# Performance work log

Hardware: AMD Instinct MI355X
Metric: run time of the kernel (lower is better)

Reference implementation:

```python
import jax, jax.numpy as jnp
import numpy as np

ALPHA = 1.0
GAMMA = 2.0
LABEL_SMOOTHING = 0.1
CENTER_W = 0.1
B, C = 32768, 1000


def setup_inputs() -> dict:
    key = jax.random.key(0)
    k1, k2 = jax.random.split(key)
    inputs = jax.random.normal(k1, (B, C), dtype=jnp.float32)
    targets = jax.random.randint(k2, (B,), 0, C, dtype=jnp.int64)
    return {"inputs": inputs, "targets": targets}


def reference(inputs, targets):
    n_classes = inputs.shape[1]
    # --- cross entropy with label smoothing (reduction='none') ---
    logp = jax.nn.log_softmax(inputs, axis=-1)                      # [B, C]
    nll = -jnp.take_along_axis(logp, targets[:, None], axis=1)[:, 0]  # [B]
    smooth = -jnp.mean(logp, axis=-1)                               # [B]
    ce = (1.0 - LABEL_SMOOTHING) * nll + LABEL_SMOOTHING * smooth
    # --- focal weighting ---
    pt = jnp.exp(-ce)
    focal = ALPHA * (1.0 - pt) ** GAMMA * ce                        # [B]
    # --- center loss (single-pass segment reduce, no per-class loop) ---
    # torch code sets centers[b, t_b] = mean_i{inputs[i, t_b] : targets[i]==t_b},
    # zero elsewhere.  sum((x - centers)^2) expands to three cheap reductions.
    gathered = jnp.take_along_axis(inputs, targets[:, None], axis=1)[:, 0]  # [B]
    sums = jax.ops.segment_sum(gathered, targets, num_segments=n_classes)
    counts = jax.ops.segment_sum(jnp.ones_like(gathered), targets,
                                 num_segments=n_classes)
    class_mean = jnp.where(counts > 0, sums / jnp.maximum(counts, 1.0), 0.0)
    m = class_mean[targets]                                          # [B]
    n_elems = inputs.shape[0] * inputs.shape[1]
    center = (jnp.sum(inputs ** 2) - 2.0 * jnp.sum(gathered * m)
              + jnp.sum(m ** 2)) / n_elems                           # scalar
    total = focal + CENTER_W * center                                # broadcast scalar
    return total.mean()
```

## Files before the change

kernel.cpp:

```cpp
#include <hip/hip_runtime.h>
#include <cmath>

#define BB 32768
#define CC 1000
#define NF4 250
#define NBLK 8192

__device__ __forceinline__ float wave_reduce_sum(float v) {
  #pragma unroll
  for (int m = 32; m >= 1; m >>= 1) v += __shfl_xor(v, m, 64);
  return v;
}
__device__ __forceinline__ float wave_reduce_max(float v) {
  #pragma unroll
  for (int m = 32; m >= 1; m >>= 1) v = fmaxf(v, __shfl_xor(v, m, 64));
  return v;
}

__global__ __launch_bounds__(256) void hfl_rows(
    const float* __restrict__ x, const int* __restrict__ tgt,
    float* __restrict__ class_sum, float* __restrict__ class_cnt,
    float* __restrict__ pfocal, float* __restrict__ ps2) {
  const int wave = threadIdx.x >> 6;
  const int lane = threadIdx.x & 63;
  const int row  = (blockIdx.x << 2) + wave;

  const float4* rp = reinterpret_cast<const float4*>(x + (size_t)row * CC);
  const int t = tgt[row];

  float4 v[4];
  bool valid[4];
  float vmax = -INFINITY;
  #pragma unroll
  for (int k = 0; k < 4; ++k) {
    const int f4 = (k << 6) + lane;
    valid[k] = (f4 < NF4);
    if (valid[k]) {
      v[k] = rp[f4];
      vmax = fmaxf(vmax, fmaxf(fmaxf(v[k].x, v[k].y), fmaxf(v[k].z, v[k].w)));
    }
  }
  const float rowmax = wave_reduce_max(vmax);

  float se = 0.f, s = 0.f, s2 = 0.f, g = 0.f;
  #pragma unroll
  for (int k = 0; k < 4; ++k) {
    if (valid[k]) {
      const int c0 = (((k << 6) + lane) << 2);
      const float a = v[k].x, b = v[k].y, c = v[k].z, d = v[k].w;
      se += __expf(a - rowmax) + __expf(b - rowmax)
          + __expf(c - rowmax) + __expf(d - rowmax);
      s  += (a + b) + (c + d);
      s2 += (a * a + b * b) + (c * c + d * d);
      if (t >= c0 && t < c0 + 4) {
        const int dd = t - c0;
        g = (dd == 0) ? a : (dd == 1) ? b : (dd == 2) ? c : d;
      }
    }
  }
  se = wave_reduce_sum(se);
  s  = wave_reduce_sum(s);
  s2 = wave_reduce_sum(s2);
  g  = wave_reduce_sum(g);

  __shared__ float sh_f[4], sh_s2[4];
  if (lane == 0) {
    const float lse = rowmax + __logf(se);
    const float ce  = lse - 0.9f * g - 0.1f * (s * (1.0f / CC));
    const float pt  = __expf(-ce);
    const float omp = 1.0f - pt;
    sh_f[wave]  = omp * omp * ce;
    sh_s2[wave] = s2;
    atomicAdd(&class_sum[t], g);
    atomicAdd(&class_cnt[t], 1.0f);
  }
  __syncthreads();
  if (threadIdx.x == 0) {
    pfocal[blockIdx.x] = (sh_f[0] + sh_f[1]) + (sh_f[2] + sh_f[3]);
    ps2[blockIdx.x]    = (sh_s2[0] + sh_s2[1]) + (sh_s2[2] + sh_s2[3]);
  }
}

__global__ __launch_bounds__(1024) void hfl_final(
    const float* __restrict__ class_sum, const float* __restrict__ class_cnt,
    const float* __restrict__ pfocal, const float* __restrict__ ps2,
    float* __restrict__ out) {
  const int tid = threadIdx.x;
  float f = 0.f, s2 = 0.f, ct = 0.f;
  #pragma unroll 2
  for (int i = tid; i < NBLK; i += 1024) { f += pfocal[i]; s2 += ps2[i]; }
  for (int c = tid; c < CC; c += 1024) {
    const float cnt = class_cnt[c];
    if (cnt > 0.f) {
      const float sm = class_sum[c];
      const float m  = sm / cnt;
      ct += 2.0f * m * sm - cnt * m * m;
    }
  }
  f  = wave_reduce_sum(f);
  s2 = wave_reduce_sum(s2);
  ct = wave_reduce_sum(ct);

  __shared__ float shf[16], shs[16], shc[16];
  const int wave = tid >> 6, lane = tid & 63;
  if (lane == 0) { shf[wave] = f; shs[wave] = s2; shc[wave] = ct; }
  __syncthreads();
  if (tid == 0) {
    float F = 0.f, S = 0.f, T = 0.f;
    #pragma unroll
    for (int w = 0; w < 16; ++w) { F += shf[w]; S += shs[w]; T += shc[w]; }
    const float center = (S - T) * (1.0f / ((float)BB * (float)CC));
    out[0] = F * (1.0f / (float)BB) + 0.1f * center;
  }
}

extern "C" void kernel_launch(void* const* d_in, const int* in_sizes, int n_in,
                              void* d_out, int out_size, void* d_ws, size_t ws_size,
                              hipStream_t stream) {
  const float* x   = (const float*)d_in[0];
  const int*   tgt = (const int*)d_in[1];
  float* out = (float*)d_out;

  float* class_sum = (float*)d_ws;
  float* class_cnt = (float*)((char*)d_ws + 4096);
  float* pfocal    = (float*)((char*)d_ws + 8192);
  float* ps2       = (float*)((char*)d_ws + 8192 + NBLK * 4);

  hipMemsetAsync(d_ws, 0, 8192, stream);

  hfl_rows<<<NBLK, 256, 0, stream>>>(x, tgt, class_sum, class_cnt, pfocal, ps2);
  hfl_final<<<1, 1024, 0, stream>>>(class_sum, class_cnt, pfocal, ps2, out);
}
```

Before: 36.09 us.

## Fuse final reduction into row kernel via last-block counter, process 4 rows per wave

Merges the separate single-block final kernel into the row kernel using an atomic block counter, so the last finishing block does the global reduction. Each wave now handles four rows instead of one, which cuts the grid to 2048 blocks and the number of partial sums. The class-center term is simplified algebraically to sum^2/count. This removes one kernel launch and its tail latency, but each wave now runs its four rows one after another, and the last block adds a serialized reduction at the end.

```diff
diff --git a/kernel.cpp b/kernel.cpp
--- a/kernel.cpp
+++ b/kernel.cpp
@@ -4,7 +4,7 @@
 #define BB 32768
 #define CC 1000
 #define NF4 250
-#define NBLK 8192
+#define NBLK 2048
 
 __device__ __forceinline__ float wave_reduce_sum(float v) {
   #pragma unroll
@@ -17,98 +17,107 @@
   return v;
 }
 
-__global__ __launch_bounds__(256) void hfl_rows(
+__global__ __launch_bounds__(256) void hfl_fused(
     const float* __restrict__ x, const int* __restrict__ tgt,
     float* __restrict__ class_sum, float* __restrict__ class_cnt,
-    float* __restrict__ pfocal, float* __restrict__ ps2) {
+    unsigned int* __restrict__ counter,
+    float* __restrict__ pfocal, float* __restrict__ ps2,
+    float* __restrict__ out) {
   const int wave = threadIdx.x >> 6;
   const int lane = threadIdx.x & 63;
-  const int row  = (blockIdx.x << 2) + wave;
 
-  const float4* rp = reinterpret_cast<const float4*>(x + (size_t)row * CC);
-  const int t = tgt[row];
+  float facc = 0.f, s2acc = 0.f;
 
-  float4 v[4];
-  bool valid[4];
-  float vmax = -INFINITY;
   #pragma unroll
-  for (int k = 0; k < 4; ++k) {
-    const int f4 = (k << 6) + lane;
-    valid[k] = (f4 < NF4);
-    if (valid[k]) {
-      v[k] = rp[f4];
-      vmax = fmaxf(vmax, fmaxf(fmaxf(v[k].x, v[k].y), fmaxf(v[k].z, v[k].w)));
-    }
-  }
-  const float rowmax = wave_reduce_max(vmax);
+  for (int j = 0; j < 4; ++j) {
+    const int row = (blockIdx.x << 4) + (wave << 2) + j;
+    const float4* rp = reinterpret_cast<const float4*>(x + (size_t)row * CC);
+    const int t = tgt[row];
 
-  float se = 0.f, s = 0.f, s2 = 0.f, g = 0.f;
-  #pragma unroll
-  for (int k = 0; k < 4; ++k) {
-    if (valid[k]) {
-      const int c0 = (((k << 6) + lane) << 2);
-      const float a = v[k].x, b = v[k].y, c = v[k].z, d = v[k].w;
-      se += __expf(a - rowmax) + __expf(b - rowmax)
-          + __expf(c - rowmax) + __expf(d - rowmax);
-      s  += (a + b) + (c + d);
-      s2 += (a * a + b * b) + (c * c + d * d);
-      if (t >= c0 && t < c0 + 4) {
-        const int dd = t - c0;
-        g = (dd == 0) ? a : (dd == 1) ? b : (dd == 2) ? c : d;
+    float4 v[4];
+    bool valid[4];
+    float vmax = -INFINITY;
+    #pragma unroll
+    for (int k = 0; k < 4; ++k) {
+      const int f4 = (k << 6) + lane;
+      valid[k] = (f4 < NF4);
+      if (valid[k]) {
+        v[k] = rp[f4];
+        vmax = fmaxf(vmax, fmaxf(fmaxf(v[k].x, v[k].y), fmaxf(v[k].z, v[k].w)));
       }
     }
-  }
-  se = wave_reduce_sum(se);
-  s  = wave_reduce_sum(s);
-  s2 = wave_reduce_sum(s2);
-  g  = wave_reduce_sum(g);
+    const float rowmax = wave_reduce_max(vmax);
 
-  __shared__ float sh_f[4], sh_s2[4];
-  if (lane == 0) {
+    float se = 0.f, s = 0.f, s2 = 0.f, g = 0.f;
+    #pragma unroll
+    for (int k = 0; k < 4; ++k) {
+      if (valid[k]) {
+        const int c0 = (((k << 6) + lane) << 2);
+        const float a = v[k].x, b = v[k].y, c = v[k].z, d = v[k].w;
+        se += __expf(a - rowmax) + __expf(b - rowmax)
+            + __expf(c - rowmax) + __expf(d - rowmax);
+        s  += (a + b) + (c + d);
+        s2 += (a * a + b * b) + (c * c + d * d);
+        if (t >= c0 && t < c0 + 4) {
+          const int dd = t - c0;
+          g = (dd == 0) ? a : (dd == 1) ? b : (dd == 2) ? c : d;
+        }
+      }
+    }
+    se = wave_reduce_sum(se);
+    s  = wave_reduce_sum(s);
+    s2 = wave_reduce_sum(s2);
+    g  = wave_reduce_sum(g);
+
     const float lse = rowmax + __logf(se);
     const float ce  = lse - 0.9f * g - 0.1f * (s * (1.0f / CC));
     const float pt  = __expf(-ce);
     const float omp = 1.0f - pt;
-    sh_f[wave]  = omp * omp * ce;
-    sh_s2[wave] = s2;
-    atomicAdd(&class_sum[t], g);
-    atomicAdd(&class_cnt[t], 1.0f);
+    facc  += omp * omp * ce;
+    s2acc += s2;
+    if (lane == 0) {
+      atomicAdd(&class_sum[t], g);
+      atomicAdd(&class_cnt[t], 1.0f);
+    }
   }
+
+  __shared__ float sh_f[4], sh_s2[4];
+  __shared__ int is_last;
+  if (lane == 0) { sh_f[wave] = facc; sh_s2[wave] = s2acc; }
   __syncthreads();
   if (threadIdx.x == 0) {
     pfocal[blockIdx.x] = (sh_f[0] + sh_f[1]) + (sh_f[2] + sh_f[3]);
     ps2[blockIdx.x]    = (sh_s2[0] + sh_s2[1]) + (sh_s2[2] + sh_s2[3]);
+    __threadfence();
+    const unsigned int old = atomicAdd(counter, 1u);
+    is_last = (old == (unsigned int)(NBLK - 1));
   }
-}
+  __syncthreads();
+  if (!is_last) return;
+  __threadfence();
 
-__global__ __launch_bounds__(1024) void hfl_final(
-    const float* __restrict__ class_sum, const float* __restrict__ class_cnt,
-    const float* __restrict__ pfocal, const float* __restrict__ ps2,
-    float* __restrict__ out) {
   const int tid = threadIdx.x;
   float f = 0.f, s2 = 0.f, ct = 0.f;
-  #pragma unroll 2
-  for (int i = tid; i < NBLK; i += 1024) { f += pfocal[i]; s2 += ps2[i]; }
-  for (int c = tid; c < CC; c += 1024) {
+  #pragma unroll 4
+  for (int i = tid; i < NBLK; i += 256) { f += pfocal[i]; s2 += ps2[i]; }
+  for (int c = tid; c < CC; c += 256) {
     const float cnt = class_cnt[c];
     if (cnt > 0.f) {
       const float sm = class_sum[c];
-      const float m  = sm / cnt;
-      ct += 2.0f * m * sm - cnt * m * m;
+      ct += sm * sm / cnt;
     }
   }
   f  = wave_reduce_sum(f);
   s2 = wave_reduce_sum(s2);
   ct = wave_reduce_sum(ct);
 
-  __shared__ float shf[16], shs[16], shc[16];
-  const int wave = tid >> 6, lane = tid & 63;
+  __shared__ float shf[4], shs[4], shc[4];
   if (lane == 0) { shf[wave] = f; shs[wave] = s2; shc[wave] = ct; }
   __syncthreads();
   if (tid == 0) {
     float F = 0.f, S = 0.f, T = 0.f;
     #pragma unroll
-    for (int w = 0; w < 16; ++w) { F += shf[w]; S += shs[w]; T += shc[w]; }
+    for (int w = 0; w < 4; ++w) { F += shf[w]; S += shs[w]; T += shc[w]; }
     const float center = (S - T) * (1.0f / ((float)BB * (float)CC));
     out[0] = F * (1.0f / (float)BB) + 0.1f * center;
   }
@@ -121,13 +130,14 @@
   const int*   tgt = (const int*)d_in[1];
   float* out = (float*)d_out;
 
-  float* class_sum = (float*)d_ws;
-  float* class_cnt = (float*)((char*)d_ws + 4096);
-  float* pfocal    = (float*)((char*)d_ws + 8192);
-  float* ps2       = (float*)((char*)d_ws + 8192 + NBLK * 4);
+  float*        class_sum = (float*)d_ws;
+  float*        class_cnt = (float*)((char*)d_ws + 4096);
+  unsigned int* counter   = (unsigned int*)((char*)d_ws + 8192);
+  float*        pfocal    = (float*)((char*)d_ws + 8448);
+  float*        ps2       = (float*)((char*)d_ws + 8448 + NBLK * 4);
 
-  hipMemsetAsync(d_ws, 0, 8192, stream);
+  hipMemsetAsync(d_ws, 0, 8448, stream);
 
-  hfl_rows<<<NBLK, 256, 0, stream>>>(x, tgt, class_sum, class_cnt, pfocal, ps2);
-  hfl_final<<<1, 1024, 0, stream>>>(class_sum, class_cnt, pfocal, ps2, out);
+  hfl_fused<<<NBLK, 256, 0, stream>>>(x, tgt, class_sum, class_cnt, counter,
+                                      pfocal, ps2, out);
 }
```

Result: slower. 92.21 us (+155.5%).
